# Optimization experiments

Hardware: AMD Instinct MI355X
Metric: run time of the kernel (lower is better)

## Reference

```python
import jax, jax.numpy as jnp
import numpy as np

N = 50000

def gcn_conv(h, W, b, src, dst, n):
    # h: [N, Fin] -> linear transform then normalized scatter-add aggregation
    h = h @ W  # [N, Fout]
    # add self-loops (PyG GCNConv default)
    loop = jnp.arange(n, dtype=src.dtype)
    s = jnp.concatenate([src, loop])
    d = jnp.concatenate([dst, loop])
    # symmetric normalization: deg^{-1/2}[s] * deg^{-1/2}[d], deg over target index
    deg = jax.ops.segment_sum(jnp.ones_like(d, dtype=h.dtype), d, num_segments=n)
    dinv = jnp.where(deg > 0, jax.lax.rsqrt(deg), 0.0)
    norm = dinv[s] * dinv[d]  # [E+N]
    msg = h[s] * norm[:, None]  # gather + scale
    out = jax.ops.segment_sum(msg, d, num_segments=n)  # scatter-add
    return out + b


def setup_inputs() -> dict:
    key = jax.random.key(0)
    k1, k2, k3, k4, k5, k6 = jax.random.split(key, 6)
    Fin, Fh, Fout = 512, 256, 64
    E = 800000
    x = jax.random.normal(k1, (N, Fin), dtype=jnp.float32)
    edge_index = jax.random.randint(k2, (2, E), 0, N, dtype=jnp.int64)
    # Glorot-style init matching nn Parameter scale
    W1 = jax.random.normal(k3, (Fin, Fh), dtype=jnp.float32) * (1.0 / np.sqrt(Fin))
    b1 = jnp.zeros((Fh,), dtype=jnp.float32)
    W2 = jax.random.normal(k4, (Fh, Fout), dtype=jnp.float32) * (1.0 / np.sqrt(Fh))
    b2 = jnp.zeros((Fout,), dtype=jnp.float32)
    return {"x": x, "edge_index": edge_index, "W1": W1, "b1": b1, "W2": W2, "b2": b2}


def reference(x, edge_index, W1, b1, W2, b2):
    src, dst = edge_index[0], edge_index[1]
    h1 = jax.nn.relu(gcn_conv(x, W1, b1, src, dst, N))
    # dropout is identity in eval mode
    h2 = gcn_conv(h1, W2, b2, src, dst, N)
    return jax.nn.log_softmax(h2, axis=1)
```

## Files before the change

kernel.cpp:

```cpp
#include <hip/hip_runtime.h>
#include <hip/hip_bf16.h>

typedef __attribute__((ext_vector_type(8))) short short8;
typedef __attribute__((ext_vector_type(4))) float f32x4;

#define NNODES 50000

__device__ __forceinline__ float b2f(unsigned short s) {
  union { unsigned int u; float f; } c; c.u = ((unsigned int)s) << 16;
  return c.f;
}
__device__ __forceinline__ unsigned short f2b(float f) {
  return __bfloat16_as_ushort(__float2bfloat16(f));
}
__device__ __forceinline__ unsigned int pkcvt(float a, float b) {
  return (unsigned int)f2b(a) | ((unsigned int)f2b(b) << 16);
}

__device__ __forceinline__ void gl_lds16(const void* g, void* l) {
  __builtin_amdgcn_global_load_lds((const __attribute__((address_space(1))) unsigned int*)g,
                                   (__attribute__((address_space(3))) unsigned int*)l, 16, 0, 0);
}

__global__ __launch_bounds__(256) void k_deg(const int* __restrict__ ei, int* __restrict__ deg, int E,
                                             int* __restrict__ rnk,
                                             const float* __restrict__ W1, const float* __restrict__ W2,
                                             unsigned short* __restrict__ w1t, unsigned short* __restrict__ w2t,
                                             const float* __restrict__ x, unsigned short* __restrict__ xb) {
  int idx = blockIdx.x * 256 + threadIdx.x;
  if (idx < E) {
    int r = atomicAdd(&deg[ei[E + idx]], 1);
    rnk[idx] = r;
  }
  if (idx < 256 * 512) { int nn = idx >> 9, kk = idx & 511; w1t[idx] = f2b(W1[kk * 256 + nn]); }
  int i2 = idx - 256 * 512;
  if (i2 >= 0 && i2 < 64 * 256) { int nn = i2 >> 8, kk = i2 & 255; w2t[i2] = f2b(W2[kk * 64 + nn]); }
  if (idx < (NNODES * 512) / 8) {
    const float4 v0 = *(const float4*)(x + (size_t)idx * 8);
    const float4 v1 = *(const float4*)(x + (size_t)idx * 8 + 4);
    uint4 p;
    p.x = pkcvt(v0.x, v0.y); p.y = pkcvt(v0.z, v0.w);
    p.z = pkcvt(v1.x, v1.y); p.w = pkcvt(v1.z, v1.w);
    *(uint4*)(xb + (size_t)idx * 8) = p;
  }
}

__global__ __launch_bounds__(256) void k_scanA(const int* __restrict__ deg, int* __restrict__ excl,
                                               int* __restrict__ blksum, float* __restrict__ dinv, int n) {
  const int i = blockIdx.x * 256 + threadIdx.x;
  const int lane = threadIdx.x & 63, wid = threadIdx.x >> 6;
  const int v = (i < n) ? deg[i] : 0;
  int x = v;
#pragma unroll
  for (int o = 1; o < 64; o <<= 1) {
    int y = __shfl_up(x, o, 64);
    if (lane >= o) x += y;
  }
  __shared__ int wsum[4];
  if (lane == 63) wsum[wid] = x;
  __syncthreads();
  int woff = 0;
  for (int w = 0; w < wid; ++w) woff += wsum[w];
  const int incl = x + woff;
  if (i < n) {
    excl[i] = incl - v;
    dinv[i] = rsqrtf((float)v + 1.0f);
  }
  if (threadIdx.x == 255) blksum[blockIdx.x] = incl;
}

__global__ __launch_bounds__(256) void k_scanC(const int* __restrict__ excl, const int* __restrict__ blksum,
                                               int* __restrict__ rowptr, int n, int E) {
  const int t = threadIdx.x;
  int partial = 0;
  for (int j = t; j < (int)blockIdx.x; j += 256) partial += blksum[j];
#pragma unroll
  for (int o = 32; o > 0; o >>= 1) partial += __shfl_xor(partial, o, 64);
  __shared__ int ws[4];
  if ((t & 63) == 0) ws[t >> 6] = partial;
  __syncthreads();
  const int off = ws[0] + ws[1] + ws[2] + ws[3];
  const int i = blockIdx.x * 256 + t;
  if (i < n) rowptr[i] = excl[i] + off;
  if (i == 0) rowptr[n] = E;
}

__global__ __launch_bounds__(256) void k_fill(const int* __restrict__ ei, const int* __restrict__ rowptr,
                                              const int* __restrict__ rnk, int* __restrict__ csr, int E) {
  int idx = blockIdx.x * 256 + threadIdx.x;
  if (idx < E) {
    const int dst = ei[E + idx];
    csr[rowptr[dst] + rnk[idx]] = ei[idx];
  }
}

__global__ __launch_bounds__(256) void k_gemm1(const unsigned short* __restrict__ xb,
    const unsigned short* __restrict__ w1t, const float* __restrict__ dinv,
    unsigned short* __restrict__ hs1b) {
  const int M = NNODES, K = 512, N = 256;
  const int NRB = (NNODES + 127) / 128;
  const int bid = blockIdx.x;
  const int rowblk = (bid >> 5) * 8 + (bid & 7);
  const int colblk = (bid >> 3) & 3;
  if (rowblk >= NRB) return;

  __shared__ unsigned short Ab[2][128][32];
  __shared__ unsigned short Bb[2][64][32];

  const int tid = threadIdx.x;
  const int w = tid >> 6, lane = tid & 63;
  const int sub = lane >> 2;
  const int brow = rowblk * 128, bcol = colblk * 64;
  const int wr = w >> 1, wc = w & 1;
  const int lr = lane & 15, lk = lane >> 4;

  const int swc = ((lane & 3) ^ ((lane >> 3) & 3)) * 8;
  const int rch = (lk ^ ((lr >> 1) & 3)) * 8;

  int gr0 = brow + w * 16 + sub;      if (gr0 >= M) gr0 = M - 1;
  int gr1 = brow + 64 + w * 16 + sub; if (gr1 >= M) gr1 = M - 1;
  const int grB = bcol + w * 16 + sub;

  const unsigned short* a0p = xb + (size_t)gr0 * K + swc;
  const unsigned short* a1p = xb + (size_t)gr1 * K + swc;
  const unsigned short* bp  = w1t + (size_t)grB * K + swc;

  f32x4 acc[4][2] = {};

#define G1_STAGE(BUF, KT) do { \
    gl_lds16(a0p + (KT), &Ab[BUF][w * 16][0]); \
    gl_lds16(a1p + (KT), &Ab[BUF][64 + w * 16][0]); \
    gl_lds16(bp  + (KT), &Bb[BUF][w * 16][0]); \
  } while (0)

  G1_STAGE(0, 0);
  G1_STAGE(1, 32);
  asm volatile("s_waitcnt vmcnt(3)" ::: "memory");
  __builtin_amdgcn_s_barrier();

  for (int s = 0; s < 16; ++s) {
    const int cur = s & 1;
    short8 af[4], bf[2];
#pragma unroll
    for (int m = 0; m < 4; ++m) af[m] = *(const short8*)&Ab[cur][wr * 64 + m * 16 + lr][rch];
#pragma unroll
    for (int n = 0; n < 2; ++n) bf[n] = *(const short8*)&Bb[cur][wc * 32 + n * 16 + lr][rch];
    if (s < 14) {
      asm volatile("s_waitcnt lgkmcnt(0)" ::: "memory");
      __builtin_amdgcn_s_barrier();
      G1_STAGE(cur, (s + 2) * 32);
    }
#pragma unroll
    for (int m = 0; m < 4; ++m)
#pragma unroll
      for (int n = 0; n < 2; ++n)
        acc[m][n] = __builtin_amdgcn_mfma_f32_16x16x32_bf16(af[m], bf[n], acc[m][n], 0, 0, 0);
    if (s < 14)      asm volatile("s_waitcnt vmcnt(3)" ::: "memory");
    else if (s == 14) asm volatile("s_waitcnt vmcnt(0)" ::: "memory");
    if (s < 15) __builtin_amdgcn_s_barrier();
  }
#undef G1_STAGE

#pragma unroll
  for (int m = 0; m < 4; ++m) {
#pragma unroll
    for (int n = 0; n < 2; ++n) {
      const int col = bcol + wc * 32 + n * 16 + lr;
#pragma unroll
      for (int j = 0; j < 4; ++j) {
        const int row = brow + wr * 64 + m * 16 + lk * 4 + j;
        if (row < M) hs1b[(size_t)row * N + col] = f2b(acc[m][n][j] * dinv[row]);
      }
    }
  }
}

__global__ __launch_bounds__(256) void k_agg1g(const int* __restrict__ rowptr,
    const int* __restrict__ csr, const unsigned short* __restrict__ hs1b,
    const float* __restrict__ dinv, const float* __restrict__ b1,
    const unsigned short* __restrict__ w2t, unsigned short* __restrict__ hs2b) {
  const int M = NNODES;
  __shared__ unsigned short h1t[16][264];
  const int tid = threadIdx.x;
  const int w = tid >> 6, lane = tid & 63;
  const int lr = lane & 15, lk = lane >> 4;
  const int brow = blockIdx.x * 16;

  const float4 bb = *(const float4*)(b1 + lane * 4);

  for (int i = 0; i < 4; ++i) {
    const int ldsrow = w * 4 + i;
    const int d = brow + ldsrow;
    f32x4 acc = {0.f, 0.f, 0.f, 0.f};
    if (d < M) {
      const int a = rowptr[d], bnd = rowptr[d + 1];
      ushort4 sv = *(const ushort4*)(hs1b + (size_t)d * 256 + lane * 4);
      acc[0] = b2f(sv.x); acc[1] = b2f(sv.y); acc[2] = b2f(sv.z); acc[3] = b2f(sv.w);
      int e = a;
      for (; e + 8 <= bnd; e += 8) {
        int s[8];
#pragma unroll
        for (int j = 0; j < 8; ++j) s[j] = csr[e + j];
        ushort4 v[8];
#pragma unroll
        for (int j = 0; j < 8; ++j) v[j] = *(const ushort4*)(hs1b + (size_t)s[j] * 256 + lane * 4);
#pragma unroll
        for (int j = 0; j < 8; ++j) {
          acc[0] += b2f(v[j].x); acc[1] += b2f(v[j].y);
          acc[2] += b2f(v[j].z); acc[3] += b2f(v[j].w);
        }
      }
      for (; e + 2 <= bnd; e += 2) {
        int s0 = csr[e], s1 = csr[e + 1];
        ushort4 v0 = *(const ushort4*)(hs1b + (size_t)s0 * 256 + lane * 4);
        ushort4 v1 = *(const ushort4*)(hs1b + (size_t)s1 * 256 + lane * 4);
        acc[0] += b2f(v0.x) + b2f(v1.x); acc[1] += b2f(v0.y) + b2f(v1.y);
        acc[2] += b2f(v0.z) + b2f(v1.z); acc[3] += b2f(v0.w) + b2f(v1.w);
      }
      for (; e < bnd; ++e) {
        int s0 = csr[e];
        ushort4 v0 = *(const ushort4*)(hs1b + (size_t)s0 * 256 + lane * 4);
        acc[0] += b2f(v0.x); acc[1] += b2f(v0.y); acc[2] += b2f(v0.z); acc[3] += b2f(v0.w);
      }
      const float di = dinv[d];
      acc[0] = fmaxf(0.f, acc[0] * di + bb.x);
      acc[1] = fmaxf(0.f, acc[1] * di + bb.y);
      acc[2] = fmaxf(0.f, acc[2] * di + bb.z);
      acc[3] = fmaxf(0.f, acc[3] * di + bb.w);
    }
    uint2 pk;
    pk.x = pkcvt(acc[0], acc[1]);
    pk.y = pkcvt(acc[2], acc[3]);
    *(uint2*)&h1t[ldsrow][lane * 4] = pk;
  }

  __syncthreads();

  f32x4 acc2 = {};
#pragma unroll
  for (int s = 0; s < 8; ++s) {
    short8 af = *(const short8*)&h1t[lr][s * 32 + lk * 8];
    short8 bfv = *(const short8*)(w2t + (size_t)(w * 16 + lr) * 256 + s * 32 + lk * 8);
    acc2 = __builtin_amdgcn_mfma_f32_16x16x32_bf16(af, bfv, acc2, 0, 0, 0);
  }

  {
    const int col = w * 16 + lr;
#pragma unroll
    for (int j = 0; j < 4; ++j) {
      const int row = brow + lk * 4 + j;
      if (row < M) hs2b[(size_t)row * 64 + col] = f2b(acc2[j] * dinv[row]);
    }
  }
}

__global__ __launch_bounds__(256) void k_agg2f(const int* __restrict__ rowptr,
    const int* __restrict__ csr, const unsigned short* __restrict__ hs2b,
    const float* __restrict__ dinv, const float* __restrict__ b2,
    float* __restrict__ out) {
  const int d = blockIdx.x * 4 + (threadIdx.x >> 6);
  if (d >= NNODES) return;
  const int lane = threadIdx.x & 63;
  const int a = rowptr[d], bnd = rowptr[d + 1];

  float acc = b2f(hs2b[(size_t)d * 64 + lane]);

  int i = a;
  for (; i + 16 <= bnd; i += 16) {
    int s[16];
#pragma unroll
    for (int j = 0; j < 16; ++j) s[j] = csr[i + j];
    unsigned short v[16];
#pragma unroll
    for (int j = 0; j < 16; ++j) v[j] = hs2b[(size_t)s[j] * 64 + lane];
#pragma unroll
    for (int j = 0; j < 16; ++j) acc += b2f(v[j]);
  }
  for (; i + 4 <= bnd; i += 4) {
    int s[4];
#pragma unroll
    for (int j = 0; j < 4; ++j) s[j] = csr[i + j];
    unsigned short v[4];
#pragma unroll
    for (int j = 0; j < 4; ++j) v[j] = hs2b[(size_t)s[j] * 64 + lane];
#pragma unroll
    for (int j = 0; j < 4; ++j) acc += b2f(v[j]);
  }
  for (; i < bnd; ++i) acc += b2f(hs2b[(size_t)csr[i] * 64 + lane]);

  float v = acc * dinv[d] + b2[lane];
  float m = v;
#pragma unroll
  for (int o = 32; o > 0; o >>= 1) m = fmaxf(m, __shfl_xor(m, o, 64));
  float ex = expf(v - m);
  float s = ex;
#pragma unroll
  for (int o = 32; o > 0; o >>= 1) s += __shfl_xor(s, o, 64);
  out[(size_t)d * 64 + lane] = v - m - logf(s);
}

extern "C" void kernel_launch(void* const* d_in, const int* in_sizes, int n_in,
                              void* d_out, int out_size, void* d_ws, size_t ws_size,
                              hipStream_t stream) {
  const float* x  = (const float*)d_in[0];
  const int*   ei = (const int*)d_in[1];
  const float* W1 = (const float*)d_in[2];
  const float* b1 = (const float*)d_in[3];
  const float* W2 = (const float*)d_in[4];
  const float* b2 = (const float*)d_in[5];
  float* out = (float*)d_out;
  const int E = in_sizes[1] / 2;
  const int n = NNODES;
  const int nblk = (n + 255) / 256;

  char* ws = (char*)d_ws;
  size_t off = 0;
  auto alloc = [&](size_t bytes) { char* p = ws + off; off = (off + bytes + 255) & ~(size_t)255; return p; };
  int*            deg    = (int*)alloc((size_t)n * 4);
  float*          dinv   = (float*)alloc((size_t)n * 4);
  int*            excl   = (int*)alloc((size_t)n * 4);
  int*            blksum = (int*)alloc((size_t)nblk * 4);
  int*            rowptr = (int*)alloc((size_t)(n + 1) * 4);
  int*            rnk    = (int*)alloc((size_t)E * 4);
  int*            csr    = (int*)alloc((size_t)E * 4);
  unsigned short* w1t    = (unsigned short*)alloc(256 * 512 * 2);
  unsigned short* w2t    = (unsigned short*)alloc(64 * 256 * 2);
  unsigned short* hs1b   = (unsigned short*)alloc((size_t)n * 256 * 2);
  unsigned short* hs2b   = (unsigned short*)alloc((size_t)n * 64 * 2);
  unsigned short* xb     = (unsigned short*)alloc((size_t)n * 512 * 2);
  (void)ws_size; (void)n_in; (void)out_size;

  hipMemsetAsync(deg, 0, (size_t)n * 4, stream);
  k_deg<<<(NNODES * 512 / 8 + 255) / 256, 256, 0, stream>>>(ei, deg, E, rnk, W1, W2, w1t, w2t, x, xb);
  k_scanA<<<nblk, 256, 0, stream>>>(deg, excl, blksum, dinv, n);
  k_scanC<<<nblk, 256, 0, stream>>>(excl, blksum, rowptr, n, E);
  k_fill<<<(E + 255) / 256, 256, 0, stream>>>(ei, rowptr, rnk, csr, E);
  k_gemm1<<<49 * 32, 256, 0, stream>>>(xb, w1t, dinv, hs1b);
  k_agg1g<<<(n + 15) / 16, 256, 0, stream>>>(rowptr, csr, hs1b, dinv, b1, w2t, hs2b);
  k_agg2f<<<(n + 3) / 4, 256, 0, stream>>>(rowptr, csr, hs2b, dinv, b2, out);
}
```

Measured before the change: 211.7 us.

## Sort nodes by degree for load-balanced layer-1 aggregation blocks

Builds a degree histogram in the scan kernel, computes bin offsets in scanC, and produces a degree-descending node permutation in k_fill. k_agg1g then processes nodes in permuted order so that each 16-node block holds nodes of similar degree. The goal is to reduce wave divergence and tail imbalance in the gather loop. In exchange it adds histogram atomics, an extra memset and permutation traffic, and the hs2b writes become scattered.

```diff
diff --git a/kernel.cpp b/kernel.cpp
--- a/kernel.cpp
+++ b/kernel.cpp
@@ -46,7 +46,8 @@
 }
 
 __global__ __launch_bounds__(256) void k_scanA(const int* __restrict__ deg, int* __restrict__ excl,
-                                               int* __restrict__ blksum, float* __restrict__ dinv, int n) {
+                                               int* __restrict__ blksum, float* __restrict__ dinv,
+                                               int* __restrict__ hist, int n) {
   const int i = blockIdx.x * 256 + threadIdx.x;
   const int lane = threadIdx.x & 63, wid = threadIdx.x >> 6;
   const int v = (i < n) ? deg[i] : 0;
@@ -57,6 +58,8 @@
     if (lane >= o) x += y;
   }
   __shared__ int wsum[4];
+  __shared__ int lh[1024];
+  for (int b = threadIdx.x; b < 1024; b += 256) lh[b] = 0;
   if (lane == 63) wsum[wid] = x;
   __syncthreads();
   int woff = 0;
@@ -65,32 +68,84 @@
   if (i < n) {
     excl[i] = incl - v;
     dinv[i] = rsqrtf((float)v + 1.0f);
+    const int dg = v > 1023 ? 1023 : v;
+    atomicAdd(&lh[1023 - dg], 1);
   }
   if (threadIdx.x == 255) blksum[blockIdx.x] = incl;
+  __syncthreads();
+  for (int b = threadIdx.x; b < 1024; b += 256) {
+    int c = lh[b];
+    if (c) atomicAdd(&hist[b], c);
+  }
 }
 
 __global__ __launch_bounds__(256) void k_scanC(const int* __restrict__ excl, const int* __restrict__ blksum,
-                                               int* __restrict__ rowptr, int n, int E) {
+                                               int* __restrict__ rowptr, const int* __restrict__ hist,
+                                               int* __restrict__ binoff, int n, int E) {
   const int t = threadIdx.x;
   int partial = 0;
   for (int j = t; j < (int)blockIdx.x; j += 256) partial += blksum[j];
 #pragma unroll
   for (int o = 32; o > 0; o >>= 1) partial += __shfl_xor(partial, o, 64);
   __shared__ int ws[4];
+  __shared__ int ws2[4];
   if ((t & 63) == 0) ws[t >> 6] = partial;
   __syncthreads();
   const int off = ws[0] + ws[1] + ws[2] + ws[3];
   const int i = blockIdx.x * 256 + t;
   if (i < n) rowptr[i] = excl[i] + off;
   if (i == 0) rowptr[n] = E;
+
+  if (blockIdx.x == 0) {
+    int h[4];
+    const int base = t * 4;
+    int sum = 0;
+#pragma unroll
+    for (int j = 0; j < 4; ++j) { h[j] = hist[base + j]; sum += h[j]; }
+    int xx = sum;
+#pragma unroll
+    for (int o = 1; o < 64; o <<= 1) {
+      int y = __shfl_up(xx, o, 64);
+      if ((t & 63) >= o) xx += y;
+    }
+    if ((t & 63) == 63) ws2[t >> 6] = xx;
+    __syncthreads();
+    int woff2 = 0;
+    for (int w2 = 0; w2 < (t >> 6); ++w2) woff2 += ws2[w2];
+    int e2 = xx + woff2 - sum;
+#pragma unroll
+    for (int j = 0; j < 4; ++j) { binoff[base + j] = e2; e2 += h[j]; }
+  }
 }
 
 __global__ __launch_bounds__(256) void k_fill(const int* __restrict__ ei, const int* __restrict__ rowptr,
-                                              const int* __restrict__ rnk, int* __restrict__ csr, int E) {
+                                              const int* __restrict__ rnk, int* __restrict__ csr, int E,
+                                              const int* __restrict__ deg, int* __restrict__ binoff,
+                                              int* __restrict__ perm) {
   int idx = blockIdx.x * 256 + threadIdx.x;
   if (idx < E) {
     const int dst = ei[E + idx];
     csr[rowptr[dst] + rnk[idx]] = ei[idx];
+  }
+  if (blockIdx.x * 256 < NNODES) {
+    __shared__ int lh[1024];
+    __shared__ int lrk[256];
+    for (int b = threadIdx.x; b < 1024; b += 256) lh[b] = 0;
+    __syncthreads();
+    const int node = blockIdx.x * 256 + threadIdx.x;
+    int bin = -1;
+    if (node < NNODES) {
+      int dg = deg[node]; if (dg > 1023) dg = 1023;
+      bin = 1023 - dg;
+      lrk[threadIdx.x] = atomicAdd(&lh[bin], 1);
+    }
+    __syncthreads();
+    for (int b = threadIdx.x; b < 1024; b += 256) {
+      int c = lh[b];
+      lh[b] = c ? atomicAdd(&binoff[b], c) : 0;
+    }
+    __syncthreads();
+    if (node < NNODES) perm[lh[bin] + lrk[threadIdx.x]] = node;
   }
 }
 
@@ -178,19 +233,27 @@
 __global__ __launch_bounds__(256) void k_agg1g(const int* __restrict__ rowptr,
     const int* __restrict__ csr, const unsigned short* __restrict__ hs1b,
     const float* __restrict__ dinv, const float* __restrict__ b1,
-    const unsigned short* __restrict__ w2t, unsigned short* __restrict__ hs2b) {
+    const unsigned short* __restrict__ w2t, const int* __restrict__ perm,
+    unsigned short* __restrict__ hs2b) {
   const int M = NNODES;
   __shared__ unsigned short h1t[16][264];
+  __shared__ int pm[16];
   const int tid = threadIdx.x;
   const int w = tid >> 6, lane = tid & 63;
   const int lr = lane & 15, lk = lane >> 4;
   const int brow = blockIdx.x * 16;
 
+  if (tid < 16) {
+    const int idx = brow + tid;
+    pm[tid] = (idx < M) ? perm[idx] : M;
+  }
+  __syncthreads();
+
   const float4 bb = *(const float4*)(b1 + lane * 4);
 
   for (int i = 0; i < 4; ++i) {
     const int ldsrow = w * 4 + i;
-    const int d = brow + ldsrow;
+    const int d = pm[ldsrow];
     f32x4 acc = {0.f, 0.f, 0.f, 0.f};
     if (d < M) {
       const int a = rowptr[d], bnd = rowptr[d + 1];
@@ -248,7 +311,7 @@
     const int col = w * 16 + lr;
 #pragma unroll
     for (int j = 0; j < 4; ++j) {
-      const int row = brow + lk * 4 + j;
+      const int row = pm[lk * 4 + j];
       if (row < M) hs2b[(size_t)row * 64 + col] = f2b(acc2[j] * dinv[row]);
     }
   }
@@ -323,6 +386,9 @@
   int*            rowptr = (int*)alloc((size_t)(n + 1) * 4);
   int*            rnk    = (int*)alloc((size_t)E * 4);
   int*            csr    = (int*)alloc((size_t)E * 4);
+  int*            hist   = (int*)alloc(1024 * 4);
+  int*            binoff = (int*)alloc(1024 * 4);
+  int*            perm   = (int*)alloc((size_t)n * 4);
   unsigned short* w1t    = (unsigned short*)alloc(256 * 512 * 2);
   unsigned short* w2t    = (unsigned short*)alloc(64 * 256 * 2);
   unsigned short* hs1b   = (unsigned short*)alloc((size_t)n * 256 * 2);
@@ -331,11 +397,12 @@
   (void)ws_size; (void)n_in; (void)out_size;
 
   hipMemsetAsync(deg, 0, (size_t)n * 4, stream);
+  hipMemsetAsync(hist, 0, 1024 * 4, stream);
   k_deg<<<(NNODES * 512 / 8 + 255) / 256, 256, 0, stream>>>(ei, deg, E, rnk, W1, W2, w1t, w2t, x, xb);
-  k_scanA<<<nblk, 256, 0, stream>>>(deg, excl, blksum, dinv, n);
-  k_scanC<<<nblk, 256, 0, stream>>>(excl, blksum, rowptr, n, E);
-  k_fill<<<(E + 255) / 256, 256, 0, stream>>>(ei, rowptr, rnk, csr, E);
+  k_scanA<<<nblk, 256, 0, stream>>>(deg, excl, blksum, dinv, hist, n);
+  k_scanC<<<nblk, 256, 0, stream>>>(excl, blksum, rowptr, hist, binoff, n, E);
+  k_fill<<<(E + 255) / 256, 256, 0, stream>>>(ei, rowptr, rnk, csr, E, deg, binoff, perm);
   k_gemm1<<<49 * 32, 256, 0, stream>>>(xb, w1t, dinv, hs1b);
-  k_agg1g<<<(n + 15) / 16, 256, 0, stream>>>(rowptr, csr, hs1b, dinv, b1, w2t, hs2b);
+  k_agg1g<<<(n + 15) / 16, 256, 0, stream>>>(rowptr, csr, hs1b, dinv, b1, w2t, perm, hs2b);
   k_agg2f<<<(n + 3) / 4, 256, 0, stream>>>(rowptr, csr, hs2b, dinv, b2, out);
 }
```

Measured after the change: 217.7 us. +2.9%, slower.
